# Performance work log

Measured on AMD Instinct MI355X. Metric: run time of the kernel, lower is better.

The kernel has to match this reference:

```python
import jax, jax.numpy as jnp
import numpy as np

N = 50000      # nodes
E = 600000     # edges
G = 64         # graphs in batch
H = 128        # hidden_dim
HEADS = 4
OUT = H // HEADS   # 32 per-head out dim
L = 3          # num GAT layers
NEG_SLOPE = 0.2    # DGL GATConv leaky_relu slope
NUM_GATES = 32
MAX_QUBITS = 20


def setup_inputs() -> dict:
    key = jax.random.key(0)
    ks = jax.random.split(key, 20)
    s = 0.05
    return {
        "gate_types": jax.random.randint(ks[0], (N,), 0, NUM_GATES),
        "qubit_indices": jax.random.randint(ks[1], (N,), 0, MAX_QUBITS),
        "src": jax.random.randint(ks[2], (E,), 0, N),
        "dst": jax.random.randint(ks[3], (E,), 0, N),
        "graph_ids": jnp.sort(jax.random.randint(ks[4], (N,), 0, G)),
        "gate_emb": jax.random.normal(ks[5], (NUM_GATES, H), jnp.float32) * s,
        "qubit_emb": jax.random.normal(ks[6], (MAX_QUBITS, H), jnp.float32) * s,
        "W": jax.random.normal(ks[7], (L, H, HEADS * OUT), jnp.float32) * s,
        "attn_l": jax.random.normal(ks[8], (L, HEADS, OUT), jnp.float32) * s,
        "attn_r": jax.random.normal(ks[9], (L, HEADS, OUT), jnp.float32) * s,
        "bias": jnp.zeros((L, HEADS * OUT), jnp.float32),
        "ln_gamma": jnp.ones((H,), jnp.float32),
        "ln_beta": jnp.zeros((H,), jnp.float32),
        "gate_w": jax.random.normal(ks[10], (H, 1), jnp.float32) * s,
        "gate_b": jnp.zeros((1,), jnp.float32),
        "proj_w1": jax.random.normal(ks[11], (H, H), jnp.float32) * s,
        "proj_b1": jnp.zeros((H,), jnp.float32),
        "proj_w2": jax.random.normal(ks[12], (H, 64), jnp.float32) * s,
        "proj_b2": jnp.zeros((64,), jnp.float32),
    }


def _segment_softmax(e, seg, num_segments):
    # numerically-stable softmax of e over groups given by seg (per row of e's axis 0)
    m = jax.ops.segment_max(e, seg, num_segments=num_segments)
    a = jnp.exp(e - m[seg])
    z = jax.ops.segment_sum(a, seg, num_segments=num_segments)
    return a / z[seg]


def _forward(gate_types, qubit_indices, src, dst, graph_ids,
             gate_emb, qubit_emb, W, attn_l, attn_r, bias,
             ln_gamma, ln_beta, gate_w, gate_b,
             proj_w1, proj_b1, proj_w2, proj_b2):
    # node embeddings (dropout layers are in eval mode -> identity)
    h = gate_emb[gate_types] + qubit_emb[qubit_indices]            # [N, H]
    for l in range(L):
        feat = (h @ W[l]).reshape(N, HEADS, OUT)                   # [N, heads, out]
        el = jnp.einsum("nho,ho->nh", feat, attn_l[l])             # [N, heads]
        er = jnp.einsum("nho,ho->nh", feat, attn_r[l])
        e = jax.nn.leaky_relu(el[src] + er[dst], NEG_SLOPE)        # [E, heads]
        a = _segment_softmax(e, dst, N)                            # edge softmax per dst node
        msg = a[:, :, None] * feat[src]                            # [E, heads, out]
        rst = jax.ops.segment_sum(msg, dst, num_segments=N)        # [N, heads, out]
        # residual: in_feats == heads*out_feats -> identity res_fc
        rst = rst + h.reshape(N, HEADS, OUT) + bias[l].reshape(1, HEADS, OUT)
        h = jax.nn.relu(rst.reshape(N, H))
    # LayerNorm
    mu = jnp.mean(h, axis=-1, keepdims=True)
    var = jnp.var(h, axis=-1, keepdims=True)
    h = (h - mu) * jax.lax.rsqrt(var + 1e-5) * ln_gamma + ln_beta
    # GlobalAttentionPooling: softmax(gate) per graph, weighted node sum
    gate = h @ gate_w + gate_b                                     # [N, 1]
    a_pool = _segment_softmax(gate, graph_ids, G)                  # [N, 1]
    z_graph = jax.ops.segment_sum(a_pool * h, graph_ids, num_segments=G)  # [G, H]
    # projection MLP
    z = jax.nn.relu(z_graph @ proj_w1 + proj_b1)
    return z @ proj_w2 + proj_b2                                   # [G, 64]


def reference(gate_types, qubit_indices, src, dst, graph_ids,
              gate_emb, qubit_emb, W, attn_l, attn_r, bias,
              ln_gamma, ln_beta, gate_w, gate_b,
              proj_w1, proj_b1, proj_w2, proj_b2):
    return _forward(gate_types, qubit_indices, src, dst, graph_ids,
                    gate_emb, qubit_emb, W, attn_l, attn_r, bias,
                    ln_gamma, ln_beta, gate_w, gate_b,
                    proj_w1, proj_b1, proj_w2, proj_b2)
```

## Files before the change

kernel.cpp:

```cpp
#include <hip/hip_runtime.h>
#include <hip/hip_bf16.h>
#include <hip/hip_fp8.h>

#define NN 50000
#define NE 600000
#define NG 64
#define HD 128
#define NL 3
#define NEG 0.2f
#define PCHUNK 16
#define SBLK 256
#define NSB ((NN + SBLK - 1) / SBLK)
#define GBLK ((NN + 63) / 64)

typedef __hip_bfloat16 bf16;
typedef unsigned short u16;
typedef unsigned int u32;
typedef unsigned char u8;
typedef __attribute__((ext_vector_type(8))) short short8v;
typedef __attribute__((ext_vector_type(4))) float float4v;
typedef __attribute__((ext_vector_type(2))) float float2v;

#define OFF_GE    0
#define OFF_QE    4096
#define OFF_W     6656
#define OFF_AL    55808
#define OFF_AR    56192
#define OFF_BIAS  56576
#define OFF_LNG   56960
#define OFF_LNB   57088
#define OFF_GW    57216
#define OFF_GB    57344
#define OFF_PW1   57345
#define OFF_PB1   73729
#define OFF_PW2   73857
#define OFF_PB2   82049
#define CVT_TOTAL 82113

__device__ __forceinline__ float b2f(bf16 x) { return __bfloat162float(x); }
__device__ __forceinline__ bf16 f2b(float x) { return __float2bfloat16(x); }
__device__ __forceinline__ float lrelu(float x) { return x > 0.f ? x : NEG * x; }
__device__ __forceinline__ float bf16lo(u32 u) { return __uint_as_float(u << 16); }
__device__ __forceinline__ float bf16hi(u32 u) { return __uint_as_float(u & 0xffff0000u); }
__device__ __forceinline__ u32 packbf16(float x, float y) {
    bf16 bx = f2b(x), by = f2b(y);
    u16 ux = *reinterpret_cast<u16*>(&bx);
    u16 uy = *reinterpret_cast<u16*>(&by);
    return (u32)ux | ((u32)uy << 16);
}

__device__ __forceinline__ u16 enc2fp8(float a, float b) {
#if __has_builtin(__builtin_amdgcn_cvt_pk_fp8_f32)
    return (u16)__builtin_amdgcn_cvt_pk_fp8_f32(a, b, 0, false);
#else
    __hip_fp8_e4m3 fa(a), fb(b);
    return (u16)fa.__x | ((u16)fb.__x << 8);
#endif
}
__device__ __forceinline__ void dec4fp8(u32 v, float& x0, float& x1,
                                        float& x2, float& x3) {
#if __has_builtin(__builtin_amdgcn_cvt_pk_f32_fp8)
    float2v lo = __builtin_amdgcn_cvt_pk_f32_fp8((int)v, false);
    float2v hi = __builtin_amdgcn_cvt_pk_f32_fp8((int)v, true);
    x0 = lo[0]; x1 = lo[1]; x2 = hi[0]; x3 = hi[1];
#else
    __hip_fp8_e4m3 t0, t1, t2, t3;
    t0.__x = v & 0xff; t1.__x = (v >> 8) & 0xff;
    t2.__x = (v >> 16) & 0xff; t3.__x = (v >> 24) & 0xff;
    x0 = (float)t0; x1 = (float)t1; x2 = (float)t2; x3 = (float)t3;
#endif
}

__device__ __forceinline__ float wave_sum64(float v) {
    #pragma unroll
    for (int m = 1; m < 64; m <<= 1) v += __shfl_xor(v, m, 64);
    return v;
}
__device__ __forceinline__ float grp_sum32(float v) {
    #pragma unroll
    for (int m = 1; m < 32; m <<= 1) v += __shfl_xor(v, m, 64);
    return v;
}

__global__ void k_diag(float* out, int n, float code) {
    int i = blockIdx.x * blockDim.x + threadIdx.x;
    if (i < n) out[i] = code;
}

struct CvtSrc { const void* p[14]; };

__global__ __launch_bounds__(256) void k_convert(CvtSrc srcs,
                                                 float* __restrict__ dst,
                                                 bf16* __restrict__ wbt,
                                                 int* __restrict__ deg) {
    __shared__ int cnt;
    if (threadIdx.x == 0) cnt = 0;
    __syncthreads();
    const u16* wraw = (const u16*)srcs.p[2];
    int bad = 0;
    for (int i = threadIdx.x; i < 2048; i += 256) {
        int e = (wraw[i] >> 7) & 0xFF;
        if (e == 0xFF || e >= 0x90) bad++;
    }
    if (bad) atomicAdd(&cnt, bad);
    __syncthreads();
    const bool isf32 = cnt > 16;

    const int starts[15] = {OFF_GE, OFF_QE, OFF_W, OFF_AL, OFF_AR, OFF_BIAS,
                            OFF_LNG, OFF_LNB, OFF_GW, OFF_GB, OFF_PW1, OFF_PB1,
                            OFF_PW2, OFF_PB2, CVT_TOTAL};
    for (int i = blockIdx.x * blockDim.x + threadIdx.x; i < CVT_TOTAL;
         i += gridDim.x * blockDim.x) {
        int a = 0;
        while (i >= starts[a + 1]) a++;
        int off = i - starts[a];
        dst[i] = isf32 ? ((const float*)srcs.p[a])[off]
                       : b2f(((const bf16*)srcs.p[a])[off]);
    }
    for (int i = blockIdx.x * blockDim.x + threadIdx.x; i < NL * HD * HD;
         i += gridDim.x * blockDim.x) {
        int l = i >> 14, rem = i & 16383;
        int col = rem >> 7, k = rem & 127;
        int si = l * 16384 + k * 128 + col;
        float v = isf32 ? ((const float*)srcs.p[2])[si]
                        : b2f(((const bf16*)srcs.p[2])[si]);
        wbt[i] = f2b(v);
    }
    for (int i = blockIdx.x * blockDim.x + threadIdx.x; i < NN;
         i += gridDim.x * blockDim.x)
        deg[i] = 0;
}

__global__ void k_embed(const int* __restrict__ gt, const int* __restrict__ qi,
                        const float* __restrict__ wc, bf16* __restrict__ h,
                        const int* __restrict__ dst, int* __restrict__ deg) {
    int idx = blockIdx.x * blockDim.x + threadIdx.x;
    if (idx < NE) atomicAdd(&deg[dst[idx]], 1);
    if (idx >= NN * 64) return;
    int n = idx >> 6, c = (idx & 63) * 2;
    int g = gt[n], q = qi[n];
    float a0 = wc[OFF_GE + g * HD + c]     + wc[OFF_QE + q * HD + c];
    float a1 = wc[OFF_GE + g * HD + c + 1] + wc[OFF_QE + q * HD + c + 1];
    *reinterpret_cast<u32*>(h + n * HD + c) = packbf16(a0, a1);
}

__global__ __launch_bounds__(SBLK) void k_bsum(const int* __restrict__ deg,
                                               int* __restrict__ bsum) {
    __shared__ int red[SBLK];
    int i = blockIdx.x * SBLK + threadIdx.x;
    red[threadIdx.x] = (i < NN) ? deg[i] : 0;
    __syncthreads();
    for (int off = SBLK / 2; off; off >>= 1) {
        if (threadIdx.x < off) red[threadIdx.x] += red[threadIdx.x + off];
        __syncthreads();
    }
    if (threadIdx.x == 0) bsum[blockIdx.x] = red[0];
}

__global__ __launch_bounds__(SBLK) void k_bscan(const int* __restrict__ bsum,
                                                int* __restrict__ boff,
                                                int* __restrict__ row_ptr) {
    __shared__ int s[SBLK];
    int t = threadIdx.x;
    int x = (t < NSB) ? bsum[t] : 0;
    s[t] = x;
    __syncthreads();
    #pragma unroll
    for (int off = 1; off < SBLK; off <<= 1) {
        int v = (t >= off) ? s[t - off] : 0;
        __syncthreads();
        if (t >= off) s[t] += v;
        __syncthreads();
    }
    if (t < NSB) boff[t] = s[t] - x;
    if (t == 0) row_ptr[NN] = s[SBLK - 1];
}

__global__ __launch_bounds__(SBLK) void k_locscan(const int* __restrict__ deg,
                                                  const int* __restrict__ boff,
                                                  int* __restrict__ row_ptr,
                                                  int* __restrict__ cursor) {
    __shared__ int s[SBLK];
    int t = threadIdx.x;
    int i = blockIdx.x * SBLK + t;
    int x = (i < NN) ? deg[i] : 0;
    s[t] = x;
    __syncthreads();
    #pragma unroll
    for (int off = 1; off < SBLK; off <<= 1) {
        int v = (t >= off) ? s[t - off] : 0;
        __syncthreads();
        if (t >= off) s[t] += v;
        __syncthreads();
    }
    if (i < NN) {
        int excl = boff[blockIdx.x] + s[t] - x;
        row_ptr[i] = excl;
        cursor[i] = excl;
    }
}

__global__ void k_fill(const int* __restrict__ src, const int* __restrict__ dst,
                       int* __restrict__ cursor, int* __restrict__ csr_src) {
    int e = blockIdx.x * blockDim.x + threadIdx.x;
    if (e < NE) {
        int p = atomicAdd(&cursor[dst[e]], 1);
        csr_src[p] = src[e];
    }
}

__global__ __launch_bounds__(256) void k_gemm_elr(
        const bf16* __restrict__ h, const bf16* __restrict__ wbt,
        const float* __restrict__ wc, u8* __restrict__ feat8,
        float* __restrict__ el, float* __restrict__ er, int l) {
    const int lane = threadIdx.x & 63, wid = threadIdx.x >> 6;
    const int r = lane & 15, q = lane >> 4;
    const int wbase = wid * 32;
    const bf16* Wt = wbt + l * HD * HD;

    short8v bfr[2][4];
    #pragma unroll
    for (int t = 0; t < 2; t++)
        #pragma unroll
        for (int ks = 0; ks < 4; ks++)
            bfr[t][ks] = *reinterpret_cast<const short8v*>(
                Wt + (wbase + 2 * r + t) * HD + ks * 32 + q * 8);

    const float al0 = wc[OFF_AL + l * HD + wbase + 2 * r];
    const float al1 = wc[OFF_AL + l * HD + wbase + 2 * r + 1];
    const float ar0 = wc[OFF_AR + l * HD + wbase + 2 * r];
    const float ar1 = wc[OFF_AR + l * HD + wbase + 2 * r + 1];

    const int base0 = blockIdx.x * 64;
    #pragma unroll
    for (int mt = 0; mt < 4; mt++) {
        const int base = base0 + mt * 16;
        if (base >= NN) break;
        float4v acc0 = {0.f, 0.f, 0.f, 0.f};
        float4v acc1 = {0.f, 0.f, 0.f, 0.f};
        #pragma unroll
        for (int ks = 0; ks < 4; ks++) {
            short8v a = *reinterpret_cast<const short8v*>(
                h + (base + r) * HD + ks * 32 + q * 8);
            acc0 = __builtin_amdgcn_mfma_f32_16x16x32_bf16(a, bfr[0][ks], acc0, 0, 0, 0);
            acc1 = __builtin_amdgcn_mfma_f32_16x16x32_bf16(a, bfr[1][ks], acc1, 0, 0, 0);
        }
        #pragma unroll
        for (int reg = 0; reg < 4; reg++) {
            const int row = base + q * 4 + reg;
            *reinterpret_cast<u16*>(feat8 + row * HD + wbase + 2 * r) =
                enc2fp8(acc0[reg], acc1[reg]);
            float elp = acc0[reg] * al0 + acc1[reg] * al1;
            float erp = acc0[reg] * ar0 + acc1[reg] * ar1;
            #pragma unroll
            for (int m = 1; m < 16; m <<= 1) {
                elp += __shfl_xor(elp, m, 64);
                erp += __shfl_xor(erp, m, 64);
            }
            if (r == 0) {
                el[row * 4 + wid] = elp;
                er[row * 4 + wid] = erp;
            }
        }
    }
}

template <bool LAST>
__global__ __launch_bounds__(256) void k_agg6(
        const u8* __restrict__ feat8, const float* __restrict__ el4,
        const float* __restrict__ er4, const int* __restrict__ row_ptr,
        const int* __restrict__ csr_src, const float* __restrict__ wc,
        bf16* __restrict__ h, float* __restrict__ gate, int l) {
    int lane = threadIdx.x & 63, wid = threadIdx.x >> 6;
    const int cL = lane & 31;
    const int p = lane >> 5;
    const int hq = cL >> 3;
    const int cb = cL * 4;
    for (int n = blockIdx.x * 4 + wid; n < NN; n += gridDim.x * 4) {
        int rp = row_ptr[n];
        int deg = row_ptr[n + 1] - rp;
        float ern = er4[n * 4 + hq];
        float a0 = 0.f, a1 = 0.f, a2 = 0.f, a3 = 0.f, z = 0.f;
        #pragma unroll 4
        for (int j = p; j < deg; j += 2) {
            int s = csr_src[rp + j];
            float elv = el4[s * 4 + hq];
            float w = __expf(lrelu(elv + ern));
            u32 f = *reinterpret_cast<const u32*>(feat8 + s * HD + cb);
            float x0, x1, x2, x3;
            dec4fp8(f, x0, x1, x2, x3);
            a0 += w * x0;
            a1 += w * x1;
            a2 += w * x2;
            a3 += w * x3;
            z += w;
        }
        a0 += __shfl_xor(a0, 32, 64);
        a1 += __shfl_xor(a1, 32, 64);
        a2 += __shfl_xor(a2, 32, 64);
        a3 += __shfl_xor(a3, 32, 64);
        z  += __shfl_xor(z, 32, 64);
        if (p == 0) {
            float inv = (deg && z != 0.f) ? 1.0f / z : 0.f;
            uint2 hv = *reinterpret_cast<const uint2*>(h + n * HD + cb);
            float v0 = fmaxf(a0 * inv + bf16lo(hv.x) + wc[OFF_BIAS + l * HD + cb], 0.f);
            float v1 = fmaxf(a1 * inv + bf16hi(hv.x) + wc[OFF_BIAS + l * HD + cb + 1], 0.f);
            float v2 = fmaxf(a2 * inv + bf16lo(hv.y) + wc[OFF_BIAS + l * HD + cb + 2], 0.f);
            float v3 = fmaxf(a3 * inv + bf16hi(hv.y) + wc[OFF_BIAS + l * HD + cb + 3], 0.f);
            if (!LAST) {
                uint2 o;
                o.x = packbf16(v0, v1);
                o.y = packbf16(v2, v3);
                *reinterpret_cast<uint2*>(h + n * HD + cb) = o;
            } else {
                float mu = grp_sum32(v0 + v1 + v2 + v3) * (1.0f / 128.0f);
                float d0 = v0 - mu, d1 = v1 - mu, d2 = v2 - mu, d3 = v3 - mu;
                float var = grp_sum32(d0 * d0 + d1 * d1 + d2 * d2 + d3 * d3)
                            * (1.0f / 128.0f);
                float rs = rsqrtf(var + 1e-5f);
                float y0 = d0 * rs * wc[OFF_LNG + cb]     + wc[OFF_LNB + cb];
                float y1 = d1 * rs * wc[OFF_LNG + cb + 1] + wc[OFF_LNB + cb + 1];
                float y2 = d2 * rs * wc[OFF_LNG + cb + 2] + wc[OFF_LNB + cb + 2];
                float y3 = d3 * rs * wc[OFF_LNG + cb + 3] + wc[OFF_LNB + cb + 3];
                uint2 o;
                o.x = packbf16(y0, y1);
                o.y = packbf16(y2, y3);
                *reinterpret_cast<uint2*>(h + n * HD + cb) = o;
                float gd = y0 * wc[OFF_GW + cb]     + y1 * wc[OFF_GW + cb + 1] +
                           y2 * wc[OFF_GW + cb + 2] + y3 * wc[OFF_GW + cb + 3];
                gd = grp_sum32(gd);
                if (lane == 0) gate[n] = gd + wc[OFF_GB];
            }
        }
    }
}

__global__ __launch_bounds__(256) void k_gmaxz(
        const float* __restrict__ gate, const int* __restrict__ gid,
        float* __restrict__ gmax, float* __restrict__ gzinv,
        int* __restrict__ gb, float* __restrict__ zg) {
    __shared__ float red[256];
    __shared__ int sb[2];
    int g = blockIdx.x, tid = threadIdx.x;
    if (tid < 2) {
        int target = g + tid;
        int lo = 0, hi = NN;
        while (lo < hi) {
            int mid = (lo + hi) >> 1;
            if (gid[mid] < target) lo = mid + 1;
            else hi = mid;
        }
        sb[tid] = lo;
        if (tid == 0) gb[g] = lo;
        if (tid == 1 && g == NG - 1) gb[NG] = lo;
    }
    if (tid < HD) zg[g * HD + tid] = 0.f;
    __syncthreads();
    int s0 = sb[0], e0 = sb[1];
    float m = -1e30f;
    for (int i = s0 + tid; i < e0; i += 256) m = fmaxf(m, gate[i]);
    red[tid] = m;
    __syncthreads();
    for (int off = 128; off; off >>= 1) {
        if (tid < off) red[tid] = fmaxf(red[tid], red[tid + off]);
        __syncthreads();
    }
    m = red[0];
    __syncthreads();
    float z = 0.f;
    for (int i = s0 + tid; i < e0; i += 256) z += __expf(gate[i] - m);
    red[tid] = z;
    __syncthreads();
    for (int off = 128; off; off >>= 1) {
        if (tid < off) red[tid] += red[tid + off];
        __syncthreads();
    }
    if (tid == 0) {
        gmax[g] = m;
        gzinv[g] = (e0 > s0 && red[0] > 0.f) ? 1.0f / red[0] : 0.f;
    }
}

__global__ __launch_bounds__(256) void k_poolsum(
        const bf16* __restrict__ h, const float* __restrict__ gate,
        const int* __restrict__ gb, const float* __restrict__ gmax,
        float* __restrict__ zg) {
    __shared__ float red[256];
    int b = blockIdx.x;
    int g = b / PCHUNK, c = b % PCHUNK;
    int s0 = gb[g], e0 = gb[g + 1];
    int len = e0 - s0;
    int beg = s0 + (int)(((long long)len * c) / PCHUNK);
    int end = s0 + (int)(((long long)len * (c + 1)) / PCHUNK);
    int ch = threadIdx.x & 127, half = threadIdx.x >> 7;
    float m = gmax[g];
    float acc = 0.f;
    for (int i = beg + half; i < end; i += 2)
        acc += __expf(gate[i] - m) * b2f(h[i * HD + ch]);
    red[threadIdx.x] = acc;
    __syncthreads();
    if (threadIdx.x < 128) {
        float v = red[threadIdx.x] + red[threadIdx.x + 128];
        if (v != 0.f) atomicAdd(&zg[g * HD + ch], v);
    }
}

__global__ __launch_bounds__(128) void k_mlp(
        const float* __restrict__ zg, const float* __restrict__ gzinv,
        const float* __restrict__ wc, float* __restrict__ out) {
    __shared__ float zr[HD], z1[HD];
    int g = blockIdx.x, tid = threadIdx.x;
    zr[tid] = zg[g * HD + tid] * gzinv[g];
    __syncthreads();
    float acc = wc[OFF_PB1 + tid];
    for (int k = 0; k < HD; k++) acc += zr[k] * wc[OFF_PW1 + k * HD + tid];
    z1[tid] = fmaxf(acc, 0.f);
    __syncthreads();
    if (tid < 64) {
        float a2 = wc[OFF_PB2 + tid];
        for (int k = 0; k < HD; k++) a2 += z1[k] * wc[OFF_PW2 + k * 64 + tid];
        out[g * 64 + tid] = a2;
    }
}

extern "C" void kernel_launch(void* const* d_in, const int* in_sizes, int n_in,
                              void* d_out, int out_size, void* d_ws, size_t ws_size,
                              hipStream_t stream) {
    const int* gate_types = (const int*)d_in[0];
    const int* qubit_idx  = (const int*)d_in[1];
    const int* src        = (const int*)d_in[2];
    const int* dst        = (const int*)d_in[3];
    const int* graph_ids  = (const int*)d_in[4];
    float* out = (float*)d_out;

    const int expect[19] = {NN, NN, NE, NE, NN, 4096, 2560, 49152, 384, 384,
                            384, 128, 128, 128, 1, 16384, 128, 8192, 64};
    for (int i = 0; i < 19 && i < n_in; i++) {
        if (in_sizes[i] != expect[i]) {
            k_diag<<<(out_size + 255) / 256, 256, 0, stream>>>(out, out_size,
                                                               7777000.f + i);
            return;
        }
    }

    char* ws = (char*)d_ws;
    size_t off = 0;
    auto alloc = [&](size_t bytes) {
        void* p = ws + off;
        off = (off + bytes + 255) & ~(size_t)255;
        return p;
    };
    float*  wc      = (float*)alloc(sizeof(float) * CVT_TOTAL);
    bf16*   wbt     = (bf16*)alloc(sizeof(bf16) * NL * HD * HD);
    float*  el      = (float*)alloc(sizeof(float) * NN * 4);
    float*  er      = (float*)alloc(sizeof(float) * NN * 4);
    int*    row_ptr = (int*)alloc(sizeof(int) * (NN + 1));
    int*    deg     = (int*)alloc(sizeof(int) * NN);
    int*    cursor  = (int*)alloc(sizeof(int) * NN);
    int*    csr_src = (int*)alloc(sizeof(int) * NE);
    int*    bsum    = (int*)alloc(sizeof(int) * NSB);
    int*    boff    = (int*)alloc(sizeof(int) * NSB);
    float*  gate    = (float*)alloc(sizeof(float) * NN);
    int*    gb      = (int*)alloc(sizeof(int) * (NG + 1));
    float*  zg      = (float*)alloc(sizeof(float) * NG * HD);
    float*  gmax    = (float*)alloc(sizeof(float) * NG);
    float*  gzinv   = (float*)alloc(sizeof(float) * NG);
    bf16*   h       = (bf16*)alloc(sizeof(bf16) * NN * HD);
    u8*     feat8   = (u8*)alloc(sizeof(u8) * NN * HD);

    if (off > ws_size) {
        k_diag<<<(out_size + 255) / 256, 256, 0, stream>>>(
            out, out_size, (float)(ws_size >> 10));
        return;
    }

    CvtSrc cs;
    for (int i = 0; i < 14; i++) cs.p[i] = d_in[5 + i];
    k_convert<<<256, 256, 0, stream>>>(cs, wc, wbt, deg);

    k_embed<<<(NN * 64 + 255) / 256, 256, 0, stream>>>(gate_types, qubit_idx,
                                                       wc, h, dst, deg);
    k_bsum<<<NSB, SBLK, 0, stream>>>(deg, bsum);
    k_bscan<<<1, SBLK, 0, stream>>>(bsum, boff, row_ptr);
    k_locscan<<<NSB, SBLK, 0, stream>>>(deg, boff, row_ptr, cursor);
    k_fill<<<(NE + 255) / 256, 256, 0, stream>>>(src, dst, cursor, csr_src);

    for (int l = 0; l < NL; l++) {
        k_gemm_elr<<<GBLK, 256, 0, stream>>>(h, wbt, wc, feat8, el, er, l);
        if (l < NL - 1)
            k_agg6<false><<<2048, 256, 0, stream>>>(feat8, el, er, row_ptr,
                                                    csr_src, wc, h, gate, l);
        else
            k_agg6<true><<<2048, 256, 0, stream>>>(feat8, el, er, row_ptr,
                                                   csr_src, wc, h, gate, l);
    }
    k_gmaxz<<<NG, 256, 0, stream>>>(gate, graph_ids, gmax, gzinv, gb, zg);
    k_poolsum<<<NG * PCHUNK, 256, 0, stream>>>(h, gate, gb, gmax, zg);
    k_mlp<<<NG, 128, 0, stream>>>(zg, gzinv, wc, out);
}
```

Before: 252.2 us.

## Assign one 32-lane group per node in GAT aggregation, merge scan kernels, enlarge GEMM tiles

```diff
diff --git a/kernel.cpp b/kernel.cpp
--- a/kernel.cpp
+++ b/kernel.cpp
@@ -11,7 +11,7 @@
 #define PCHUNK 16
 #define SBLK 256
 #define NSB ((NN + SBLK - 1) / SBLK)
-#define GBLK ((NN + 63) / 64)
+#define GBLK2 ((NN + 127) / 128)
 
 typedef __hip_bfloat16 bf16;
 typedef unsigned short u16;
@@ -71,11 +71,6 @@
 #endif
 }
 
-__device__ __forceinline__ float wave_sum64(float v) {
-    #pragma unroll
-    for (int m = 1; m < 64; m <<= 1) v += __shfl_xor(v, m, 64);
-    return v;
-}
 __device__ __forceinline__ float grp_sum32(float v) {
     #pragma unroll
     for (int m = 1; m < 32; m <<= 1) v += __shfl_xor(v, m, 64);
@@ -157,12 +152,26 @@
     if (threadIdx.x == 0) bsum[blockIdx.x] = red[0];
 }
 
-__global__ __launch_bounds__(SBLK) void k_bscan(const int* __restrict__ bsum,
-                                                int* __restrict__ boff,
-                                                int* __restrict__ row_ptr) {
+__global__ __launch_bounds__(SBLK) void k_locscan(const int* __restrict__ deg,
+                                                  const int* __restrict__ bsum,
+                                                  int* __restrict__ row_ptr,
+                                                  int* __restrict__ cursor) {
     __shared__ int s[SBLK];
+    __shared__ int boffs;
     int t = threadIdx.x;
-    int x = (t < NSB) ? bsum[t] : 0;
+    int part = (t < NSB && t < blockIdx.x) ? bsum[t] : 0;
+    #pragma unroll
+    for (int m = 1; m < 64; m <<= 1) part += __shfl_xor(part, m, 64);
+    if (t == 0) s[0] = 0;
+    __syncthreads();
+    if ((t & 63) == 0) atomicAdd(&s[0], part);
+    __syncthreads();
+    if (t == 0) boffs = s[0];
+    __syncthreads();
+    int boff = boffs;
+
+    int i = blockIdx.x * SBLK + t;
+    int x = (i < NN) ? deg[i] : 0;
     s[t] = x;
     __syncthreads();
     #pragma unroll
@@ -172,32 +181,13 @@
         if (t >= off) s[t] += v;
         __syncthreads();
     }
-    if (t < NSB) boff[t] = s[t] - x;
-    if (t == 0) row_ptr[NN] = s[SBLK - 1];
-}
-
-__global__ __launch_bounds__(SBLK) void k_locscan(const int* __restrict__ deg,
-                                                  const int* __restrict__ boff,
-                                                  int* __restrict__ row_ptr,
-                                                  int* __restrict__ cursor) {
-    __shared__ int s[SBLK];
-    int t = threadIdx.x;
-    int i = blockIdx.x * SBLK + t;
-    int x = (i < NN) ? deg[i] : 0;
-    s[t] = x;
-    __syncthreads();
-    #pragma unroll
-    for (int off = 1; off < SBLK; off <<= 1) {
-        int v = (t >= off) ? s[t - off] : 0;
-        __syncthreads();
-        if (t >= off) s[t] += v;
-        __syncthreads();
-    }
     if (i < NN) {
-        int excl = boff[blockIdx.x] + s[t] - x;
+        int excl = boff + s[t] - x;
         row_ptr[i] = excl;
         cursor[i] = excl;
     }
+    if (blockIdx.x == NSB - 1 && t == SBLK - 1)
+        row_ptr[NN] = boff + s[t];
 }
 
 __global__ void k_fill(const int* __restrict__ src, const int* __restrict__ dst,
@@ -231,9 +221,9 @@
     const float ar0 = wc[OFF_AR + l * HD + wbase + 2 * r];
     const float ar1 = wc[OFF_AR + l * HD + wbase + 2 * r + 1];
 
-    const int base0 = blockIdx.x * 64;
+    const int base0 = blockIdx.x * 128;
     #pragma unroll
-    for (int mt = 0; mt < 4; mt++) {
+    for (int mt = 0; mt < 8; mt++) {
         const int base = base0 + mt * 16;
         if (base >= NN) break;
         float4v acc0 = {0.f, 0.f, 0.f, 0.f};
@@ -266,23 +256,23 @@
 }
 
 template <bool LAST>
-__global__ __launch_bounds__(256) void k_agg6(
+__global__ __launch_bounds__(256) void k_agg7(
         const u8* __restrict__ feat8, const float* __restrict__ el4,
         const float* __restrict__ er4, const int* __restrict__ row_ptr,
         const int* __restrict__ csr_src, const float* __restrict__ wc,
         bf16* __restrict__ h, float* __restrict__ gate, int l) {
-    int lane = threadIdx.x & 63, wid = threadIdx.x >> 6;
-    const int cL = lane & 31;
-    const int p = lane >> 5;
-    const int hq = cL >> 3;
-    const int cb = cL * 4;
-    for (int n = blockIdx.x * 4 + wid; n < NN; n += gridDim.x * 4) {
+    int tid = threadIdx.x;
+    const int grp = tid >> 5;
+    const int gl = tid & 31;
+    const int hq = gl >> 3;
+    const int cb = gl * 4;
+    for (int n = blockIdx.x * 8 + grp; n < NN; n += gridDim.x * 8) {
         int rp = row_ptr[n];
         int deg = row_ptr[n + 1] - rp;
         float ern = er4[n * 4 + hq];
         float a0 = 0.f, a1 = 0.f, a2 = 0.f, a3 = 0.f, z = 0.f;
         #pragma unroll 4
-        for (int j = p; j < deg; j += 2) {
+        for (int j = 0; j < deg; j++) {
             int s = csr_src[rp + j];
             float elv = el4[s * 4 + hq];
             float w = __expf(lrelu(elv + ern));
@@ -295,42 +285,35 @@
             a3 += w * x3;
             z += w;
         }
-        a0 += __shfl_xor(a0, 32, 64);
-        a1 += __shfl_xor(a1, 32, 64);
-        a2 += __shfl_xor(a2, 32, 64);
-        a3 += __shfl_xor(a3, 32, 64);
-        z  += __shfl_xor(z, 32, 64);
-        if (p == 0) {
-            float inv = (deg && z != 0.f) ? 1.0f / z : 0.f;
-            uint2 hv = *reinterpret_cast<const uint2*>(h + n * HD + cb);
-            float v0 = fmaxf(a0 * inv + bf16lo(hv.x) + wc[OFF_BIAS + l * HD + cb], 0.f);
-            float v1 = fmaxf(a1 * inv + bf16hi(hv.x) + wc[OFF_BIAS + l * HD + cb + 1], 0.f);
-            float v2 = fmaxf(a2 * inv + bf16lo(hv.y) + wc[OFF_BIAS + l * HD + cb + 2], 0.f);
-            float v3 = fmaxf(a3 * inv + bf16hi(hv.y) + wc[OFF_BIAS + l * HD + cb + 3], 0.f);
-            if (!LAST) {
-                uint2 o;
-                o.x = packbf16(v0, v1);
-                o.y = packbf16(v2, v3);
-                *reinterpret_cast<uint2*>(h + n * HD + cb) = o;
-            } else {
-                float mu = grp_sum32(v0 + v1 + v2 + v3) * (1.0f / 128.0f);
-                float d0 = v0 - mu, d1 = v1 - mu, d2 = v2 - mu, d3 = v3 - mu;
-                float var = grp_sum32(d0 * d0 + d1 * d1 + d2 * d2 + d3 * d3)
-                            * (1.0f / 128.0f);
-                float rs = rsqrtf(var + 1e-5f);
-                float y0 = d0 * rs * wc[OFF_LNG + cb]     + wc[OFF_LNB + cb];
-                float y1 = d1 * rs * wc[OFF_LNG + cb + 1] + wc[OFF_LNB + cb + 1];
-                float y2 = d2 * rs * wc[OFF_LNG + cb + 2] + wc[OFF_LNB + cb + 2];
-                float y3 = d3 * rs * wc[OFF_LNG + cb + 3] + wc[OFF_LNB + cb + 3];
-                uint2 o;
-                o.x = packbf16(y0, y1);
-                o.y = packbf16(y2, y3);
-                *reinterpret_cast<uint2*>(h + n * HD + cb) = o;
-                float gd = y0 * wc[OFF_GW + cb]     + y1 * wc[OFF_GW + cb + 1] +
-                           y2 * wc[OFF_GW + cb + 2] + y3 * wc[OFF_GW + cb + 3];
-                gd = grp_sum32(gd);
-                if (lane == 0) gate[n] = gd + wc[OFF_GB];
-            }
+        float inv = (deg && z != 0.f) ? 1.0f / z : 0.f;
+        uint2 hv = *reinterpret_cast<const uint2*>(h + n * HD + cb);
+        float v0 = fmaxf(a0 * inv + bf16lo(hv.x) + wc[OFF_BIAS + l * HD + cb], 0.f);
+        float v1 = fmaxf(a1 * inv + bf16hi(hv.x) + wc[OFF_BIAS + l * HD + cb + 1], 0.f);
+        float v2 = fmaxf(a2 * inv + bf16lo(hv.y) + wc[OFF_BIAS + l * HD + cb + 2], 0.f);
+        float v3 = fmaxf(a3 * inv + bf16hi(hv.y) + wc[OFF_BIAS + l * HD + cb + 3], 0.f);
+        if (!LAST) {
+            uint2 o;
+            o.x = packbf16(v0, v1);
+            o.y = packbf16(v2, v3);
+            *reinterpret_cast<uint2*>(h + n * HD + cb) = o;
+        } else {
+            float mu = grp_sum32(v0 + v1 + v2 + v3) * (1.0f / 128.0f);
+            float d0 = v0 - mu, d1 = v1 - mu, d2 = v2 - mu, d3 = v3 - mu;
+            float var = grp_sum32(d0 * d0 + d1 * d1 + d2 * d2 + d3 * d3)
+                        * (1.0f / 128.0f);
+            float rs = rsqrtf(var + 1e-5f);
+            float y0 = d0 * rs * wc[OFF_LNG + cb]     + wc[OFF_LNB + cb];
+            float y1 = d1 * rs * wc[OFF_LNG + cb + 1] + wc[OFF_LNB + cb + 1];
+            float y2 = d2 * rs * wc[OFF_LNG + cb + 2] + wc[OFF_LNB + cb + 2];
+            float y3 = d3 * rs * wc[OFF_LNG + cb + 3] + wc[OFF_LNB + cb + 3];
+            uint2 o;
+            o.x = packbf16(y0, y1);
+            o.y = packbf16(y2, y3);
+            *reinterpret_cast<uint2*>(h + n * HD + cb) = o;
+            float gd = y0 * wc[OFF_GW + cb]     + y1 * wc[OFF_GW + cb + 1] +
+                       y2 * wc[OFF_GW + cb + 2] + y3 * wc[OFF_GW + cb + 3];
+            gd = grp_sum32(gd);
+            if (gl == 0) gate[n] = gd + wc[OFF_GB];
         }
     }
 }
@@ -459,7 +442,6 @@
     int*    cursor  = (int*)alloc(sizeof(int) * NN);
     int*    csr_src = (int*)alloc(sizeof(int) * NE);
     int*    bsum    = (int*)alloc(sizeof(int) * NSB);
-    int*    boff    = (int*)alloc(sizeof(int) * NSB);
     float*  gate    = (float*)alloc(sizeof(float) * NN);
     int*    gb      = (int*)alloc(sizeof(int) * (NG + 1));
     float*  zg      = (float*)alloc(sizeof(float) * NG * HD);
@@ -481,17 +463,16 @@
     k_embed<<<(NN * 64 + 255) / 256, 256, 0, stream>>>(gate_types, qubit_idx,
                                                        wc, h, dst, deg);
     k_bsum<<<NSB, SBLK, 0, stream>>>(deg, bsum);
-    k_bscan<<<1, SBLK, 0, stream>>>(bsum, boff, row_ptr);
-    k_locscan<<<NSB, SBLK, 0, stream>>>(deg, boff, row_ptr, cursor);
+    k_locscan<<<NSB, SBLK, 0, stream>>>(deg, bsum, row_ptr, cursor);
     k_fill<<<(NE + 255) / 256, 256, 0, stream>>>(src, dst, cursor, csr_src);
 
     for (int l = 0; l < NL; l++) {
-        k_gemm_elr<<<GBLK, 256, 0, stream>>>(h, wbt, wc, feat8, el, er, l);
+        k_gemm_elr<<<GBLK2, 256, 0, stream>>>(h, wbt, wc, feat8, el, er, l);
         if (l < NL - 1)
-            k_agg6<false><<<2048, 256, 0, stream>>>(feat8, el, er, row_ptr,
+            k_agg7<false><<<2048, 256, 0, stream>>>(feat8, el, er, row_ptr,
                                                     csr_src, wc, h, gate, l);
         else
-            k_agg6<true><<<2048, 256, 0, stream>>>(feat8, el, er, row_ptr,
+            k_agg7<true><<<2048, 256, 0, stream>>>(feat8, el, er, row_ptr,
                                                    csr_src, wc, h, gate, l);
     }
     k_gmaxz<<<NG, 256, 0, stream>>>(gate, graph_ids, gmax, gzinv, gb, zg);
```

Result: faster. 246.7 us (-2.2%).
